# Performance work log

Measured on AMD Instinct MI355X. Metric: run time of the kernel, lower is better.

The kernel has to match this reference:

```python
import jax, jax.numpy as jnp
import numpy as np

N_NODES = 20000
N_EDGES = 320000
IN_DIM = 64        # 18 + 7 + 19 + 20
EDGE_DIM0 = 112    # edge_length of conv1
HID = 50
N_REST = 9         # conv2..conv10
EPS = 1e-5


def setup_inputs() -> dict:
    key = jax.random.key(0)
    ks = jax.random.split(key, 16)
    s = 0.05
    x = jax.random.normal(ks[0], (N_NODES, IN_DIM), jnp.float32)
    edge_index = jax.random.randint(ks[1], (2, N_EDGES), 0, N_NODES, jnp.int32)
    edge_attr = jax.random.normal(ks[2], (N_EDGES, EDGE_DIM0), jnp.float32)
    distance = jax.random.normal(ks[3], (N_EDGES,), jnp.float32)
    d1 = 2 * IN_DIM + EDGE_DIM0       # concat width for layer 1
    dk = 2 * HID + HID                # concat width for layers 2..10
    return {
        "x": x,
        "edge_index": edge_index,
        "edge_attr": edge_attr,
        "distance": distance,
        # layer-1 params (edge-conditioned message MLP + edge-update MLP)
        "W1m": jax.random.normal(ks[4], (d1, HID), jnp.float32) * s,
        "b1m": jnp.zeros((HID,), jnp.float32),
        "W1e": jax.random.normal(ks[5], (d1, HID), jnp.float32) * s,
        "b1e": jnp.zeros((HID,), jnp.float32),
        "g1": jnp.ones((HID,), jnp.float32),
        "bt1": jnp.zeros((HID,), jnp.float32),
        # layers 2..10, stacked
        "Wm": jax.random.normal(ks[6], (N_REST, dk, HID), jnp.float32) * s,
        "bm": jnp.zeros((N_REST, HID), jnp.float32),
        "We": jax.random.normal(ks[7], (N_REST, dk, HID), jnp.float32) * s,
        "be": jnp.zeros((N_REST, HID), jnp.float32),
        "gam": jnp.ones((N_REST, HID), jnp.float32),
        "bet": jnp.zeros((N_REST, HID), jnp.float32),
    }


def reference(x, edge_index, edge_attr, distance,
              W1m, b1m, W1e, b1e, g1, bt1,
              Wm, bm, We, be, gam, bet):
    src = edge_index[0]
    dst = edge_index[1]

    def gcn(xn, ea, Wm_, bm_, We_, be_):
        # gather endpoint features, concat with edge_attr: [E, 2*F + Fe]
        h = jnp.concatenate([xn[dst], xn[src], ea], axis=-1)
        m = h @ Wm_ + bm_                 # per-edge message   [E, HID]
        e_new = h @ We_ + be_             # updated edge_attr  [E, HID]
        xo = jax.ops.segment_sum(m, dst, num_segments=N_NODES)  # scatter-add
        return xo, e_new

    def bn(v, g, b):
        # BatchNorm1d, batch-statistics (training-mode) semantics
        mu = v.mean(0)
        var = ((v - mu) ** 2).mean(0)
        return (v - mu) * jax.lax.rsqrt(var + EPS) * g + b

    x1, e = gcn(x, edge_attr, W1m, b1m, W1e, b1e)
    x1 = jax.nn.elu(bn(x1, g1, bt1))
    cur = x1  # cumulative residual sum x1 + x2 + ... + xk
    for i in range(N_REST):
        xi, e = gcn(cur, e, Wm[i], bm[i], We[i], be[i])
        xi = jax.nn.elu(bn(xi, gam[i], bet[i]))
        cur = cur + xi
    return cur  # x10_C: [N_NODES, HID]
```

## Files before the change

kernel.cpp:

```cpp
#include <hip/hip_runtime.h>
#include <hip/hip_bf16.h>
#include <math.h>

#define N_NODES 20000
#define N_EDGES 320000
#define HID 50
#define XS 64

typedef short bf16x8 __attribute__((ext_vector_type(8)));
typedef float f32x4 __attribute__((ext_vector_type(4)));

__device__ inline ushort f2bf(float f) {
    __hip_bfloat16 h = __float2bfloat16(f);
    union { __hip_bfloat16 h; ushort u; } c; c.h = h; return c.u;
}
__device__ inline uint pack2(float a, float b) {
    return (uint)f2bf(a) | ((uint)f2bf(b) << 16);
}

__device__ inline void lds_barrier() {
    asm volatile("s_waitcnt lgkmcnt(0)" ::: "memory");
    __builtin_amdgcn_sched_barrier(0);
    __builtin_amdgcn_s_barrier();
    __builtin_amdgcn_sched_barrier(0);
    asm volatile("" ::: "memory");
}

__global__ __launch_bounds__(256) void hist_kernel(const int* __restrict__ dst, int* __restrict__ cnt) {
    const int e = blockIdx.x * 256 + threadIdx.x;
    if (e < N_EDGES) atomicAdd(&cnt[dst[e]], 1);
}

__global__ __launch_bounds__(1024) void scan_kernel(const int* __restrict__ cnt, int* __restrict__ offs) {
    __shared__ int part[1024];
    const int t = threadIdx.x;
    int loc[20]; int s = 0;
    #pragma unroll
    for (int i = 0; i < 20; ++i) {
        const int idx = t * 20 + i;
        const int v = (idx < N_NODES) ? cnt[idx] : 0;
        loc[i] = s; s += v;
    }
    part[t] = s; __syncthreads();
    for (int off = 1; off < 1024; off <<= 1) {
        const int v = (t >= off) ? part[t - off] : 0;
        __syncthreads();
        part[t] += v;
        __syncthreads();
    }
    const int ex = (t > 0) ? part[t - 1] : 0;
    #pragma unroll
    for (int i = 0; i < 20; ++i) {
        const int idx = t * 20 + i;
        if (idx < N_NODES) offs[idx] = ex + loc[i];
    }
}

__global__ __launch_bounds__(256) void scatter_kernel(const int* __restrict__ src, const int* __restrict__ dst,
        int* __restrict__ offs, int* __restrict__ perm,
        int* __restrict__ sdst_p, int* __restrict__ ssrc_p) {
    const int e = blockIdx.x * 256 + threadIdx.x;
    if (e >= N_EDGES) return;
    const int d = dst[e];
    const int pos = atomicAdd(&offs[d], 1);
    perm[pos] = e;
    sdst_p[pos] = d;
    ssrc_p[pos] = src[e];
}

__global__ __launch_bounds__(256) void xconv_kernel(const float* __restrict__ x, ushort* __restrict__ xb1) {
    const int i = blockIdx.x * 256 + threadIdx.x;
    if (i < N_NODES * 64) xb1[i] = f2bf(x[i]);
}

__global__ __launch_bounds__(256) void prep_w_kernel(
    const float* __restrict__ Wm, const float* __restrict__ We,
    const float* __restrict__ bm, const float* __restrict__ be,
    ushort* __restrict__ Wt, float* __restrict__ bc, int F, int FE, int Kpad)
{
    const int l = blockIdx.y;
    const int K = 2 * F + FE;
    const float* Wm_l = Wm + (size_t)l * K * HID;
    const float* We_l = We + (size_t)l * K * HID;
    const float* bm_l = bm + (size_t)l * HID;
    const float* be_l = be + (size_t)l * HID;
    ushort* Wt_l = Wt + (size_t)l * 128 * Kpad;
    float*  bc_l = bc + (size_t)l * 128;
    for (int idx = blockIdx.x * 256 + threadIdx.x; idx < 128 * Kpad; idx += gridDim.x * 256) {
        const int c = idx / Kpad;
        const int k = idx - c * Kpad;
        int r = -1;
        if (k < 64)       { if (k < F)        r = k; }
        else if (k < 128) { if (k - 64 < F)   r = F + (k - 64); }
        else              { if (k - 128 < FE) r = 2 * F + (k - 128); }
        float v = 0.f;
        if (r >= 0) {
            if (c < HID)                      v = Wm_l[(size_t)r * HID + c];
            else if (c >= 64 && c < 64 + HID) v = We_l[(size_t)r * HID + (c - 64)];
        }
        Wt_l[(size_t)c * Kpad + k] = f2bf(v);
        if (k == 0) {
            float b = 0.f;
            if (c < HID)                      b = bm_l[c];
            else if (c >= 64 && c < 64 + HID) b = be_l[c - 64];
            bc_l[c] = b;
        }
    }
}

template<int NCH, bool L1>
__global__ __launch_bounds__(256, L1 ? 1 : 4) void msg_mfma_kernel(
    const ushort* __restrict__ xb,
    const float*  __restrict__ ea,
    const ushort* __restrict__ ein,
    const int*    __restrict__ perm,
    ushort* __restrict__ eout,
    const int* __restrict__ sdst_idx, const int* __restrict__ ssrc_idx,
    const ushort* __restrict__ Wt,
    const float* __restrict__ bc,
    float* __restrict__ xo)
{
    constexpr int KPAD = NCH * 32;
    constexpr int KPS  = KPAD + 8;
    constexpr int NT   = N_EDGES / 32;

    __shared__ __align__(16) ushort hl[32 * KPS];
    __shared__ __align__(16) float  xol[32 * 52];
    __shared__ __align__(16) ushort epack[32 * 72];
    __shared__ int sdst_s[2][32];
    __shared__ int segs[34];
    __shared__ int nseg_s;

    const int t = threadIdx.x;
    const int lane = t & 63, w = t >> 6;
    const int r = t >> 3, ch0 = t & 7;
    const int row16 = lane & 15, g = lane >> 4;
    const int G = gridDim.x;

    int sd, ss, pm;
    bf16x8 Rd, Rs, Re;
    float4 P0a, P0b, P1a, P1b;

    auto issue = [&](int tl) {
        const int eb = tl * 32;
        sd = sdst_idx[eb + r];
        ss = ssrc_idx[eb + r];
        Rd = *(const bf16x8*)(xb + (size_t)sd * XS + ch0 * 8);
        Rs = *(const bf16x8*)(xb + (size_t)ss * XS + ch0 * 8);
        if constexpr (L1) {
            pm = perm[eb + r];
            const float* pe = ea + (size_t)pm * 112;
            P0a = *(const float4*)(pe + 8 * ch0);
            P0b = *(const float4*)(pe + 8 * ch0 + 4);
            if (ch0 < 6) {
                P1a = *(const float4*)(pe + 8 * (ch0 + 8));
                P1b = *(const float4*)(pe + 8 * (ch0 + 8) + 4);
            }
        } else {
            Re = *(const bf16x8*)(ein + ((size_t)eb + r) * XS + ch0 * 8);
        }
    };

    auto write_stage = [&](int par) {
        *(bf16x8*)&hl[r * KPS + ch0 * 8]      = Rd;
        *(bf16x8*)&hl[r * KPS + 64 + ch0 * 8] = Rs;
        if constexpr (L1) {
            union { bf16x8 v; uint u[4]; } c0;
            c0.u[0] = pack2(P0a.x, P0a.y); c0.u[1] = pack2(P0a.z, P0a.w);
            c0.u[2] = pack2(P0b.x, P0b.y); c0.u[3] = pack2(P0b.z, P0b.w);
            *(bf16x8*)&hl[r * KPS + 128 + ch0 * 8] = c0.v;
            if (ch0 < 6) {
                union { bf16x8 v; uint u[4]; } c1;
                c1.u[0] = pack2(P1a.x, P1a.y); c1.u[1] = pack2(P1a.z, P1a.w);
                c1.u[2] = pack2(P1b.x, P1b.y); c1.u[3] = pack2(P1b.z, P1b.w);
                *(bf16x8*)&hl[r * KPS + 192 + ch0 * 8] = c1.v;
            } else {
                *(bf16x8*)&hl[r * KPS + 192 + ch0 * 8] = (bf16x8){0,0,0,0,0,0,0,0};
            }
        } else {
            *(bf16x8*)&hl[r * KPS + 128 + ch0 * 8] = Re;
        }
        if (ch0 == 0) sdst_s[par][r] = sd;
    };

    int tile = blockIdx.x;
    if (tile >= NT) return;

    const int colA = (2 * w) * 16 + row16;
    const int colB = colA + 16;
    const float bA = bc[colA], bB = bc[colB];
    const ushort* wpA = Wt + (size_t)colA * KPAD + 8 * g;
    const ushort* wpB = Wt + (size_t)colB * KPAD + 8 * g;

    bf16x8 BfA[NCH], BfB[NCH];
    if constexpr (!L1) {
        #pragma unroll
        for (int c = 0; c < NCH; ++c) {
            BfA[c] = *(const bf16x8*)(wpA + c * 32);
            BfB[c] = *(const bf16x8*)(wpB + c * 32);
        }
    }

    issue(tile);
    write_stage(0);
    if (tile + G < NT) issue(tile + G);
    __syncthreads();

    int par = 0;
    for (; tile < NT; tile += G) {
        f32x4 accA0 = (f32x4){bA, bA, bA, bA}, accA1 = accA0;
        f32x4 accB0 = (f32x4){bB, bB, bB, bB}, accB1 = accB0;
        #pragma unroll
        for (int c = 0; c < NCH; ++c) {
            const bf16x8 a0 = *(const bf16x8*)&hl[row16 * KPS + c * 32 + 8 * g];
            const bf16x8 a1 = *(const bf16x8*)&hl[(16 + row16) * KPS + c * 32 + 8 * g];
            bf16x8 B0, B1;
            if constexpr (L1) {
                B0 = *(const bf16x8*)(wpA + c * 32);
                B1 = *(const bf16x8*)(wpB + c * 32);
            } else {
                B0 = BfA[c];
                B1 = BfB[c];
            }
            accA0 = __builtin_amdgcn_mfma_f32_16x16x32_bf16(a0, B0, accA0, 0, 0, 0);
            accA1 = __builtin_amdgcn_mfma_f32_16x16x32_bf16(a1, B0, accA1, 0, 0, 0);
            accB0 = __builtin_amdgcn_mfma_f32_16x16x32_bf16(a0, B1, accB0, 0, 0, 0);
            accB1 = __builtin_amdgcn_mfma_f32_16x16x32_bf16(a1, B1, accB1, 0, 0, 0);
        }

        if (w < 2) {
            #pragma unroll
            for (int rr = 0; rr < 4; ++rr) {
                if (colA < HID) {
                    xol[(4 * g + rr) * 52 + colA]      = accA0[rr];
                    xol[(16 + 4 * g + rr) * 52 + colA] = accA1[rr];
                }
                if (colB < HID) {
                    xol[(4 * g + rr) * 52 + colB]      = accB0[rr];
                    xol[(16 + 4 * g + rr) * 52 + colB] = accB1[rr];
                }
            }
        } else {
            const int lcA = colA - 64, lcB = colB - 64;
            #pragma unroll
            for (int rr = 0; rr < 4; ++rr) {
                epack[(4 * g + rr) * 72 + lcA]      = f2bf(accA0[rr]);
                epack[(16 + 4 * g + rr) * 72 + lcA] = f2bf(accA1[rr]);
                epack[(4 * g + rr) * 72 + lcB]      = f2bf(accB0[rr]);
                epack[(16 + 4 * g + rr) * 72 + lcB] = f2bf(accB1[rr]);
            }
        }

        if (w == 0) {
            const int l31 = lane & 31;
            const int dl  = sdst_s[par][l31];
            const int dp  = sdst_s[par][l31 > 0 ? l31 - 1 : 0];
            const bool flag = (l31 == 0) || (dl != dp);
            const unsigned long long bal = __ballot(flag) & 0xFFFFFFFFull;
            if (lane < 32 && flag)
                segs[__popcll(bal & ((1ull << l31) - 1ull))] = l31;
            if (lane == 0) {
                const int ns = __popcll(bal);
                nseg_s = ns;
                segs[ns] = 32;
            }
        }
        lds_barrier();

        if (tile + G < NT)     write_stage(par ^ 1);
        if (tile + 2 * G < NT) issue(tile + 2 * G);

        {
            const int4 v = *(const int4*)&epack[r * 72 + ch0 * 8];
            *(int4*)&eout[((size_t)tile * 32 + r) * XS + ch0 * 8] = v;
        }
        const int ns = nseg_s;
        for (int idx = t; idx < ns * HID; idx += 256) {
            const int s = idx / HID, col = idx - s * HID;
            const int a0 = segs[s], b0 = segs[s + 1];
            float s0 = 0.f, s1 = 0.f, s2 = 0.f, s3 = 0.f;
            int rr = a0;
            for (; rr + 4 <= b0; rr += 4) {
                s0 += xol[(rr + 0) * 52 + col];
                s1 += xol[(rr + 1) * 52 + col];
                s2 += xol[(rr + 2) * 52 + col];
                s3 += xol[(rr + 3) * 52 + col];
            }
            for (; rr < b0; ++rr) s0 += xol[rr * 52 + col];
            atomicAdd(&xo[(size_t)sdst_s[par][a0] * HID + col], (s0 + s1) + (s2 + s3));
        }
        lds_barrier();
        par ^= 1;
    }
}

__global__ __launch_bounds__(256) void stats_kernel(const float* __restrict__ xo,
                                                    float* __restrict__ sacc)
{
    __shared__ float sp[5][HID], sq[5][HID];
    const int t = threadIdx.x;
    if (t < 250) {
        float s = 0.f, q = 0.f;
        const size_t base = (size_t)blockIdx.x * 12500 + t;
        #pragma unroll
        for (int it = 0; it < 50; ++it) {
            const float v = xo[base + it * 250];
            s += v; q += v * v;
        }
        sp[t / HID][t % HID] = s;
        sq[t / HID][t % HID] = q;
    }
    __syncthreads();
    if (t < HID) {
        float s = 0.f, q = 0.f;
        #pragma unroll
        for (int p = 0; p < 5; ++p) { s += sp[p][t]; q += sq[p][t]; }
        atomicAdd(&sacc[t], s);
        atomicAdd(&sacc[HID + t], q);
    }
}

template<bool FIRST>
__global__ __launch_bounds__(256) void apply_kernel(float* __restrict__ xo,
    const float* __restrict__ sacc,
    const float* __restrict__ g, const float* __restrict__ b,
    float* __restrict__ cur, ushort* __restrict__ xb)
{
    const int i = blockIdx.x * 256 + threadIdx.x;
    if (i >= N_NODES * HID) return;
    const int c = i % HID;
    const float inv = 1.f / (float)N_NODES;
    const float mu = sacc[c] * inv;
    const float var = sacc[HID + c] * inv - mu * mu;
    const float z = (xo[i] - mu) * rsqrtf(var + 1e-5f) * g[c] + b[c];
    xo[i] = 0.f;
    const float a = (z > 0.f) ? z : expm1f(z);
    const float nc = FIRST ? a : (cur[i] + a);
    cur[i] = nc;
    xb[(size_t)(i / HID) * XS + c] = f2bf(nc);
}

extern "C" void kernel_launch(void* const* d_in, const int* in_sizes, int n_in,
                              void* d_out, int out_size, void* d_ws, size_t ws_size,
                              hipStream_t stream)
{
    const float* x    = (const float*)d_in[0];
    const int*   ei   = (const int*)  d_in[1];
    const float* ea   = (const float*)d_in[2];
    const float* W1m  = (const float*)d_in[4];
    const float* b1m  = (const float*)d_in[5];
    const float* W1e  = (const float*)d_in[6];
    const float* b1e  = (const float*)d_in[7];
    const float* g1   = (const float*)d_in[8];
    const float* bt1  = (const float*)d_in[9];
    const float* Wm   = (const float*)d_in[10];
    const float* bm   = (const float*)d_in[11];
    const float* We   = (const float*)d_in[12];
    const float* be   = (const float*)d_in[13];
    const float* gam  = (const float*)d_in[14];
    const float* bet  = (const float*)d_in[15];

    float* out = (float*)d_out;

    char* ws = (char*)d_ws;
    ushort* e_ws   = (ushort*)(ws + 0);
    float*  xo     = (float*) (ws + 40960000);
    float*  sacc   = (float*) (ws + 44960000);
    ushort* Wt1    = (ushort*)(ws + 44965120);
    float*  bc1    = (float*) (ws + 45030656);
    ushort* Wtk    = (ushort*)(ws + 45031168);
    float*  bck    = (float*) (ws + 45473536);
    ushort* xb1    = (ushort*)(ws + 45478656);
    ushort* xb     = (ushort*)(ws + 48038656);
    int*    cnt    = (int*)   (ws + 50598656);
    int*    offs   = (int*)   (ws + 50678656);
    int*    perm   = (int*)   (ws + 50758656);
    int*    sdst_p = (int*)   (ws + 52038656);
    int*    ssrc_p = (int*)   (ws + 53318656);

    const int* srcs = ei;
    const int* dsts = ei + N_EDGES;
    const int nApply = (N_NODES * HID + 255) / 256;

    hipMemsetAsync(xo, 0, 4005120, stream);
    hipMemsetAsync(xb, 0, 2560000, stream);
    hipMemsetAsync(cnt, 0, N_NODES * sizeof(int), stream);
    hist_kernel<<<1250, 256, 0, stream>>>(dsts, cnt);
    scan_kernel<<<1, 1024, 0, stream>>>(cnt, offs);
    scatter_kernel<<<1250, 256, 0, stream>>>(srcs, dsts, offs, perm, sdst_p, ssrc_p);
    xconv_kernel<<<5000, 256, 0, stream>>>(x, xb1);
    prep_w_kernel<<<dim3(128, 1), 256, 0, stream>>>(W1m, W1e, b1m, b1e, Wt1, bc1, 64, 112, 256);
    prep_w_kernel<<<dim3(128, 9), 256, 0, stream>>>(Wm, We, bm, be, Wtk, bck, 50, 50, 192);

    msg_mfma_kernel<8, true>
        <<<1280, 256, 0, stream>>>(xb1, ea, (const ushort*)nullptr, perm,
                                   e_ws, sdst_p, ssrc_p, Wt1, bc1, xo);
    stats_kernel<<<80, 256, 0, stream>>>(xo, sacc);
    apply_kernel<true><<<nApply, 256, 0, stream>>>(xo, sacc, g1, bt1, out, xb);

    for (int i = 0; i < 9; ++i) {
        msg_mfma_kernel<6, false>
            <<<1024, 256, 0, stream>>>(xb, (const float*)nullptr, e_ws, (const int*)nullptr,
                                       e_ws, sdst_p, ssrc_p,
                                       Wtk + (size_t)i * 128 * 192,
                                       bck + (size_t)i * 128, xo);
        stats_kernel<<<80, 256, 0, stream>>>(xo, sacc + (i + 1) * 128);
        apply_kernel<false><<<nApply, 256, 0, stream>>>(xo, sacc + (i + 1) * 128,
                                                        gam + (size_t)i * HID,
                                                        bet + (size_t)i * HID, out, xb);
    }
}
```

Baseline: 527.0 us.

## Fuse BN stats and apply into one grid-synced kernel; prefetch indices earlier

Merges the BatchNorm statistics and apply kernels into one kernel. Each block caches its slice of the aggregated features in LDS, contributes partial sums, then spins on an atomic counter in the sacc workspace until all 250 blocks arrive, and applies BN+ELU from the cache. This removes one launch per layer and a second global read of xo. The message kernel also splits index loading from the feature gather, so indices are fetched one tile further ahead and their latency is hidden. The spin barrier only works if all 250 blocks are co-resident, and it depends on the counter slot in sacc starting at zero.

```diff
diff --git a/kernel.cpp b/kernel.cpp
--- a/kernel.cpp
+++ b/kernel.cpp
@@ -137,19 +137,23 @@
     const int row16 = lane & 15, g = lane >> 4;
     const int G = gridDim.x;
 
-    int sd, ss, pm;
+    int sdN, ssN, pmN;
+    int sdW;
     bf16x8 Rd, Rs, Re;
     float4 P0a, P0b, P1a, P1b;
 
-    auto issue = [&](int tl) {
+    auto load_idx = [&](int tl) {
         const int eb = tl * 32;
-        sd = sdst_idx[eb + r];
-        ss = ssrc_idx[eb + r];
-        Rd = *(const bf16x8*)(xb + (size_t)sd * XS + ch0 * 8);
-        Rs = *(const bf16x8*)(xb + (size_t)ss * XS + ch0 * 8);
+        sdN = sdst_idx[eb + r];
+        ssN = ssrc_idx[eb + r];
+        if constexpr (L1) pmN = perm[eb + r];
+    };
+
+    auto gather = [&](int tl) {
+        Rd = *(const bf16x8*)(xb + (size_t)sdN * XS + ch0 * 8);
+        Rs = *(const bf16x8*)(xb + (size_t)ssN * XS + ch0 * 8);
         if constexpr (L1) {
-            pm = perm[eb + r];
-            const float* pe = ea + (size_t)pm * 112;
+            const float* pe = ea + (size_t)pmN * 112;
             P0a = *(const float4*)(pe + 8 * ch0);
             P0b = *(const float4*)(pe + 8 * ch0 + 4);
             if (ch0 < 6) {
@@ -157,8 +161,9 @@
                 P1b = *(const float4*)(pe + 8 * (ch0 + 8) + 4);
             }
         } else {
-            Re = *(const bf16x8*)(ein + ((size_t)eb + r) * XS + ch0 * 8);
-        }
+            Re = *(const bf16x8*)(ein + ((size_t)tl * 32 + r) * XS + ch0 * 8);
+        }
+        sdW = sdN;
     };
 
     auto write_stage = [&](int par) {
@@ -180,7 +185,7 @@
         } else {
             *(bf16x8*)&hl[r * KPS + 128 + ch0 * 8] = Re;
         }
-        if (ch0 == 0) sdst_s[par][r] = sd;
+        if (ch0 == 0) sdst_s[par][r] = sdW;
     };
 
     int tile = blockIdx.x;
@@ -201,9 +206,9 @@
         }
     }
 
-    issue(tile);
-    write_stage(0);
-    if (tile + G < NT) issue(tile + G);
+    load_idx(tile); gather(tile); write_stage(0);
+    if (tile + G < NT)     { load_idx(tile + G); gather(tile + G); }
+    if (tile + 2 * G < NT) load_idx(tile + 2 * G);
     __syncthreads();
 
     int par = 0;
@@ -268,7 +273,8 @@
         lds_barrier();
 
         if (tile + G < NT)     write_stage(par ^ 1);
-        if (tile + 2 * G < NT) issue(tile + 2 * G);
+        if (tile + 2 * G < NT) gather(tile + 2 * G);
+        if (tile + 3 * G < NT) load_idx(tile + 3 * G);
 
         {
             const int4 v = *(const int4*)&epack[r * 72 + ch0 * 8];
@@ -294,17 +300,25 @@
     }
 }
 
-__global__ __launch_bounds__(256) void stats_kernel(const float* __restrict__ xo,
-                                                    float* __restrict__ sacc)
+template<bool FIRST>
+__global__ __launch_bounds__(256) void bnapply_kernel(float* __restrict__ xo,
+    float* __restrict__ sacc,
+    const float* __restrict__ g, const float* __restrict__ b,
+    float* __restrict__ cur, ushort* __restrict__ xb)
 {
+    __shared__ float cache[4000];
     __shared__ float sp[5][HID], sq[5][HID];
+    __shared__ float mvs[2 * HID];
+
     const int t = threadIdx.x;
+    const size_t base = (size_t)blockIdx.x * 4000;
+
     if (t < 250) {
         float s = 0.f, q = 0.f;
-        const size_t base = (size_t)blockIdx.x * 12500 + t;
         #pragma unroll
-        for (int it = 0; it < 50; ++it) {
-            const float v = xo[base + it * 250];
+        for (int it = 0; it < 16; ++it) {
+            const float v = xo[base + t + it * 250];
+            cache[t + it * 250] = v;
             s += v; q += v * v;
         }
         sp[t / HID][t % HID] = s;
@@ -318,26 +332,31 @@
         atomicAdd(&sacc[t], s);
         atomicAdd(&sacc[HID + t], q);
     }
-}
-
-template<bool FIRST>
-__global__ __launch_bounds__(256) void apply_kernel(float* __restrict__ xo,
-    const float* __restrict__ sacc,
-    const float* __restrict__ g, const float* __restrict__ b,
-    float* __restrict__ cur, ushort* __restrict__ xb)
-{
-    const int i = blockIdx.x * 256 + threadIdx.x;
-    if (i >= N_NODES * HID) return;
-    const int c = i % HID;
+    __syncthreads();
+
+    if (t == 0) {
+        int* cnt = (int*)(sacc + 112);
+        atomicAdd(cnt, 1);
+        while (atomicAdd(cnt, 0) < 250) { __builtin_amdgcn_s_sleep(8); }
+    }
+    __syncthreads();
+
+    if (t < 2 * HID) mvs[t] = atomicAdd(&sacc[t], 0.0f);
+    __syncthreads();
+
     const float inv = 1.f / (float)N_NODES;
-    const float mu = sacc[c] * inv;
-    const float var = sacc[HID + c] * inv - mu * mu;
-    const float z = (xo[i] - mu) * rsqrtf(var + 1e-5f) * g[c] + b[c];
-    xo[i] = 0.f;
-    const float a = (z > 0.f) ? z : expm1f(z);
-    const float nc = FIRST ? a : (cur[i] + a);
-    cur[i] = nc;
-    xb[(size_t)(i / HID) * XS + c] = f2bf(nc);
+    for (int i = t; i < 4000; i += 256) {
+        const int c = i % HID;
+        const int node = (int)(base / HID) + i / HID;
+        const float mu = mvs[c] * inv;
+        const float var = mvs[HID + c] * inv - mu * mu;
+        const float z = (cache[i] - mu) * rsqrtf(var + 1e-5f) * g[c] + b[c];
+        xo[base + i] = 0.f;
+        const float a = (z > 0.f) ? z : expm1f(z);
+        const float nc = FIRST ? a : (cur[base + i] + a);
+        cur[base + i] = nc;
+        xb[(size_t)node * XS + c] = f2bf(nc);
+    }
 }
 
 extern "C" void kernel_launch(void* const* d_in, const int* in_sizes, int n_in,
@@ -380,7 +399,6 @@
 
     const int* srcs = ei;
     const int* dsts = ei + N_EDGES;
-    const int nApply = (N_NODES * HID + 255) / 256;
 
     hipMemsetAsync(xo, 0, 4005120, stream);
     hipMemsetAsync(xb, 0, 2560000, stream);
@@ -395,8 +413,7 @@
     msg_mfma_kernel<8, true>
         <<<1280, 256, 0, stream>>>(xb1, ea, (const ushort*)nullptr, perm,
                                    e_ws, sdst_p, ssrc_p, Wt1, bc1, xo);
-    stats_kernel<<<80, 256, 0, stream>>>(xo, sacc);
-    apply_kernel<true><<<nApply, 256, 0, stream>>>(xo, sacc, g1, bt1, out, xb);
+    bnapply_kernel<true><<<250, 256, 0, stream>>>(xo, sacc, g1, bt1, out, xb);
 
     for (int i = 0; i < 9; ++i) {
         msg_mfma_kernel<6, false>
@@ -404,9 +421,8 @@
                                        e_ws, sdst_p, ssrc_p,
                                        Wtk + (size_t)i * 128 * 192,
                                        bck + (size_t)i * 128, xo);
-        stats_kernel<<<80, 256, 0, stream>>>(xo, sacc + (i + 1) * 128);
-        apply_kernel<false><<<nApply, 256, 0, stream>>>(xo, sacc + (i + 1) * 128,
-                                                        gam + (size_t)i * HID,
-                                                        bet + (size_t)i * HID, out, xb);
-    }
-}
+        bnapply_kernel<false><<<250, 256, 0, stream>>>(xo, sacc + (i + 1) * 128,
+                                                       gam + (size_t)i * HID,
+                                                       bet + (size_t)i * HID, out, xb);
+    }
+}
```

Result: slower. 654.0 us (+24.1%).

## Generalize edge tile size and use 64-edge tiles for layers 2-10

Applied to the files above, without the earlier changes.

Templates the message kernel on edges-per-tile so each block processes 64 edges per iteration in layers 2-10, with four M-subtiles of MFMA per B fragment and a full-wave ballot for segment detection. This reuses register-resident weights across more rows, halves per-tile barrier and loop overhead, and lets segments of equal destination span more edges so fewer atomics are issued. It also drops the occupancy hint from launch bounds and lowers the grid to 768 blocks. In exchange it raises LDS and register use per block, which may reduce occupancy, and doubles the in-flight gather registers.

```diff
diff --git a/kernel.cpp b/kernel.cpp
--- a/kernel.cpp
+++ b/kernel.cpp
@@ -108,8 +108,8 @@
     }
 }
 
-template<int NCH, bool L1>
-__global__ __launch_bounds__(256, L1 ? 1 : 4) void msg_mfma_kernel(
+template<int NCH, int ET, bool L1>
+__global__ __launch_bounds__(256) void msg_mfma_kernel(
     const ushort* __restrict__ xb,
     const float*  __restrict__ ea,
     const ushort* __restrict__ ein,
@@ -122,13 +122,15 @@
 {
     constexpr int KPAD = NCH * 32;
     constexpr int KPS  = KPAD + 8;
-    constexpr int NT   = N_EDGES / 32;
-
-    __shared__ __align__(16) ushort hl[32 * KPS];
-    __shared__ __align__(16) float  xol[32 * 52];
-    __shared__ __align__(16) ushort epack[32 * 72];
-    __shared__ int sdst_s[2][32];
-    __shared__ int segs[34];
+    constexpr int NT   = N_EDGES / ET;
+    constexpr int MT   = ET / 16;
+    constexpr int NR   = ET / 32;
+
+    __shared__ __align__(16) ushort hl[ET * KPS];
+    __shared__ __align__(16) float  xol[ET * 52];
+    __shared__ __align__(16) ushort epack[ET * 72];
+    __shared__ int sdst_s[2][ET];
+    __shared__ int segs[ET + 2];
     __shared__ int nseg_s;
 
     const int t = threadIdx.x;
@@ -137,50 +139,60 @@
     const int row16 = lane & 15, g = lane >> 4;
     const int G = gridDim.x;
 
-    int sd, ss, pm;
-    bf16x8 Rd, Rs, Re;
+    int sd[NR], ss[NR], pm[NR];
+    bf16x8 Rd[NR], Rs[NR], Re[NR];
     float4 P0a, P0b, P1a, P1b;
 
     auto issue = [&](int tl) {
-        const int eb = tl * 32;
-        sd = sdst_idx[eb + r];
-        ss = ssrc_idx[eb + r];
-        Rd = *(const bf16x8*)(xb + (size_t)sd * XS + ch0 * 8);
-        Rs = *(const bf16x8*)(xb + (size_t)ss * XS + ch0 * 8);
-        if constexpr (L1) {
-            pm = perm[eb + r];
-            const float* pe = ea + (size_t)pm * 112;
-            P0a = *(const float4*)(pe + 8 * ch0);
-            P0b = *(const float4*)(pe + 8 * ch0 + 4);
-            if (ch0 < 6) {
-                P1a = *(const float4*)(pe + 8 * (ch0 + 8));
-                P1b = *(const float4*)(pe + 8 * (ch0 + 8) + 4);
-            }
-        } else {
-            Re = *(const bf16x8*)(ein + ((size_t)eb + r) * XS + ch0 * 8);
+        #pragma unroll
+        for (int i = 0; i < NR; ++i) {
+            const int eb = tl * ET + i * 32;
+            sd[i] = sdst_idx[eb + r];
+            ss[i] = ssrc_idx[eb + r];
+            if constexpr (L1) pm[i] = perm[eb + r];
+        }
+        #pragma unroll
+        for (int i = 0; i < NR; ++i) {
+            Rd[i] = *(const bf16x8*)(xb + (size_t)sd[i] * XS + ch0 * 8);
+            Rs[i] = *(const bf16x8*)(xb + (size_t)ss[i] * XS + ch0 * 8);
+            if constexpr (L1) {
+                const float* pe = ea + (size_t)pm[i] * 112;
+                P0a = *(const float4*)(pe + 8 * ch0);
+                P0b = *(const float4*)(pe + 8 * ch0 + 4);
+                if (ch0 < 6) {
+                    P1a = *(const float4*)(pe + 8 * (ch0 + 8));
+                    P1b = *(const float4*)(pe + 8 * (ch0 + 8) + 4);
+                }
+            } else {
+                Re[i] = *(const bf16x8*)(ein + ((size_t)tl * ET + i * 32 + r) * XS + ch0 * 8);
+            }
         }
     };
 
     auto write_stage = [&](int par) {
-        *(bf16x8*)&hl[r * KPS + ch0 * 8]      = Rd;
-        *(bf16x8*)&hl[r * KPS + 64 + ch0 * 8] = Rs;
-        if constexpr (L1) {
-            union { bf16x8 v; uint u[4]; } c0;
-            c0.u[0] = pack2(P0a.x, P0a.y); c0.u[1] = pack2(P0a.z, P0a.w);
-            c0.u[2] = pack2(P0b.x, P0b.y); c0.u[3] = pack2(P0b.z, P0b.w);
-            *(bf16x8*)&hl[r * KPS + 128 + ch0 * 8] = c0.v;
-            if (ch0 < 6) {
-                union { bf16x8 v; uint u[4]; } c1;
-                c1.u[0] = pack2(P1a.x, P1a.y); c1.u[1] = pack2(P1a.z, P1a.w);
-                c1.u[2] = pack2(P1b.x, P1b.y); c1.u[3] = pack2(P1b.z, P1b.w);
-                *(bf16x8*)&hl[r * KPS + 192 + ch0 * 8] = c1.v;
+        #pragma unroll
+        for (int i = 0; i < NR; ++i) {
+            const int row = r + i * 32;
+            *(bf16x8*)&hl[row * KPS + ch0 * 8]      = Rd[i];
+            *(bf16x8*)&hl[row * KPS + 64 + ch0 * 8] = Rs[i];
+            if constexpr (L1) {
+                union { bf16x8 v; uint u[4]; } c0;
+                c0.u[0] = pack2(P0a.x, P0a.y); c0.u[1] = pack2(P0a.z, P0a.w);
+                c0.u[2] = pack2(P0b.x, P0b.y); c0.u[3] = pack2(P0b.z, P0b.w);
+                *(bf16x8*)&hl[row * KPS + 128 + ch0 * 8] = c0.v;
+                if (ch0 < 6) {
+                    union { bf16x8 v; uint u[4]; } c1;
+                    c1.u[0] = pack2(P1a.x, P1a.y); c1.u[1] = pack2(P1a.z, P1a.w);
+                    c1.u[2] = pack2(P1b.x, P1b.y); c1.u[3] = pack2(P1b.z, P1b.w);
+                    *(bf16x8*)&hl[row * KPS + 192 + ch0 * 8] = c1.v;
+                } else {
+                    *(bf16x8*)&hl[row * KPS + 192 + ch0 * 8] = (bf16x8){0,0,0,0,0,0,0,0};
+                }
             } else {
-                *(bf16x8*)&hl[r * KPS + 192 + ch0 * 8] = (bf16x8){0,0,0,0,0,0,0,0};
-            }
-        } else {
-            *(bf16x8*)&hl[r * KPS + 128 + ch0 * 8] = Re;
-        }
-        if (ch0 == 0) sdst_s[par][r] = sd;
+                *(bf16x8*)&hl[row * KPS + 128 + ch0 * 8] = Re[i];
+            }
+            if (ch0 == 0) sdst_s[par][row] = sd[i];
+        }
     };
 
     int tile = blockIdx.x;
@@ -208,12 +220,18 @@
 
     int par = 0;
     for (; tile < NT; tile += G) {
-        f32x4 accA0 = (f32x4){bA, bA, bA, bA}, accA1 = accA0;
-        f32x4 accB0 = (f32x4){bB, bB, bB, bB}, accB1 = accB0;
+        f32x4 accA[MT], accB[MT];
+        #pragma unroll
+        for (int m = 0; m < MT; ++m) {
+            accA[m] = (f32x4){bA, bA, bA, bA};
+            accB[m] = (f32x4){bB, bB, bB, bB};
+        }
         #pragma unroll
         for (int c = 0; c < NCH; ++c) {
-            const bf16x8 a0 = *(const bf16x8*)&hl[row16 * KPS + c * 32 + 8 * g];
-            const bf16x8 a1 = *(const bf16x8*)&hl[(16 + row16) * KPS + c * 32 + 8 * g];
+            bf16x8 a[MT];
+            #pragma unroll
+            for (int m = 0; m < MT; ++m)
+                a[m] = *(const bf16x8*)&hl[(m * 16 + row16) * KPS + c * 32 + 8 * g];
             bf16x8 B0, B1;
             if constexpr (L1) {
                 B0 = *(const bf16x8*)(wpA + c * 32);
@@ -222,47 +240,61 @@
                 B0 = BfA[c];
                 B1 = BfB[c];
             }
-            accA0 = __builtin_amdgcn_mfma_f32_16x16x32_bf16(a0, B0, accA0, 0, 0, 0);
-            accA1 = __builtin_amdgcn_mfma_f32_16x16x32_bf16(a1, B0, accA1, 0, 0, 0);
-            accB0 = __builtin_amdgcn_mfma_f32_16x16x32_bf16(a0, B1, accB0, 0, 0, 0);
-            accB1 = __builtin_amdgcn_mfma_f32_16x16x32_bf16(a1, B1, accB1, 0, 0, 0);
+            #pragma unroll
+            for (int m = 0; m < MT; ++m) {
+                accA[m] = __builtin_amdgcn_mfma_f32_16x16x32_bf16(a[m], B0, accA[m], 0, 0, 0);
+                accB[m] = __builtin_amdgcn_mfma_f32_16x16x32_bf16(a[m], B1, accB[m], 0, 0, 0);
+            }
         }
 
         if (w < 2) {
             #pragma unroll
-            for (int rr = 0; rr < 4; ++rr) {
-                if (colA < HID) {
-                    xol[(4 * g + rr) * 52 + colA]      = accA0[rr];
-                    xol[(16 + 4 * g + rr) * 52 + colA] = accA1[rr];
-                }
-                if (colB < HID) {
-                    xol[(4 * g + rr) * 52 + colB]      = accB0[rr];
-                    xol[(16 + 4 * g + rr) * 52 + colB] = accB1[rr];
+            for (int m = 0; m < MT; ++m) {
+                #pragma unroll
+                for (int rr = 0; rr < 4; ++rr) {
+                    const int row = m * 16 + 4 * g + rr;
+                    if (colA < HID) xol[row * 52 + colA] = accA[m][rr];
+                    if (colB < HID) xol[row * 52 + colB] = accB[m][rr];
                 }
             }
         } else {
             const int lcA = colA - 64, lcB = colB - 64;
             #pragma unroll
-            for (int rr = 0; rr < 4; ++rr) {
-                epack[(4 * g + rr) * 72 + lcA]      = f2bf(accA0[rr]);
-                epack[(16 + 4 * g + rr) * 72 + lcA] = f2bf(accA1[rr]);
-                epack[(4 * g + rr) * 72 + lcB]      = f2bf(accB0[rr]);
-                epack[(16 + 4 * g + rr) * 72 + lcB] = f2bf(accB1[rr]);
+            for (int m = 0; m < MT; ++m) {
+                #pragma unroll
+                for (int rr = 0; rr < 4; ++rr) {
+                    const int row = m * 16 + 4 * g + rr;
+                    epack[row * 72 + lcA] = f2bf(accA[m][rr]);
+                    epack[row * 72 + lcB] = f2bf(accB[m][rr]);
+                }
             }
         }
 
         if (w == 0) {
-            const int l31 = lane & 31;
-            const int dl  = sdst_s[par][l31];
-            const int dp  = sdst_s[par][l31 > 0 ? l31 - 1 : 0];
-            const bool flag = (l31 == 0) || (dl != dp);
-            const unsigned long long bal = __ballot(flag) & 0xFFFFFFFFull;
-            if (lane < 32 && flag)
-                segs[__popcll(bal & ((1ull << l31) - 1ull))] = l31;
-            if (lane == 0) {
-                const int ns = __popcll(bal);
-                nseg_s = ns;
-                segs[ns] = 32;
+            if constexpr (ET == 64) {
+                const int dl = sdst_s[par][lane];
+                const int dp = sdst_s[par][lane > 0 ? lane - 1 : 0];
+                const bool flag = (lane == 0) || (dl != dp);
+                const unsigned long long bal = __ballot(flag);
+                if (flag) segs[__popcll(bal & ((1ull << lane) - 1ull))] = lane;
+                if (lane == 63) {
+                    const int ns = __popcll(bal);
+                    nseg_s = ns;
+                    segs[ns] = 64;
+                }
+            } else {
+                const int l31 = lane & 31;
+                const int dl  = sdst_s[par][l31];
+                const int dp  = sdst_s[par][l31 > 0 ? l31 - 1 : 0];
+                const bool flag = (l31 == 0) || (dl != dp);
+                const unsigned long long bal = __ballot(flag) & 0xFFFFFFFFull;
+                if (lane < 32 && flag)
+                    segs[__popcll(bal & ((1ull << l31) - 1ull))] = l31;
+                if (lane == 0) {
+                    const int ns = __popcll(bal);
+                    nseg_s = ns;
+                    segs[ns] = 32;
+                }
             }
         }
         lds_barrier();
@@ -270,9 +302,11 @@
         if (tile + G < NT)     write_stage(par ^ 1);
         if (tile + 2 * G < NT) issue(tile + 2 * G);
 
-        {
-            const int4 v = *(const int4*)&epack[r * 72 + ch0 * 8];
-            *(int4*)&eout[((size_t)tile * 32 + r) * XS + ch0 * 8] = v;
+        #pragma unroll
+        for (int i = 0; i < NR; ++i) {
+            const int row = r + i * 32;
+            const int4 v = *(const int4*)&epack[row * 72 + ch0 * 8];
+            *(int4*)&eout[((size_t)tile * ET + row) * XS + ch0 * 8] = v;
         }
         const int ns = nseg_s;
         for (int idx = t; idx < ns * HID; idx += 256) {
@@ -392,18 +426,18 @@
     prep_w_kernel<<<dim3(128, 1), 256, 0, stream>>>(W1m, W1e, b1m, b1e, Wt1, bc1, 64, 112, 256);
     prep_w_kernel<<<dim3(128, 9), 256, 0, stream>>>(Wm, We, bm, be, Wtk, bck, 50, 50, 192);
 
-    msg_mfma_kernel<8, true>
+    msg_mfma_kernel<8, 32, true>
         <<<1280, 256, 0, stream>>>(xb1, ea, (const ushort*)nullptr, perm,
                                    e_ws, sdst_p, ssrc_p, Wt1, bc1, xo);
     stats_kernel<<<80, 256, 0, stream>>>(xo, sacc);
     apply_kernel<true><<<nApply, 256, 0, stream>>>(xo, sacc, g1, bt1, out, xb);
 
     for (int i = 0; i < 9; ++i) {
-        msg_mfma_kernel<6, false>
-            <<<1024, 256, 0, stream>>>(xb, (const float*)nullptr, e_ws, (const int*)nullptr,
-                                       e_ws, sdst_p, ssrc_p,
-                                       Wtk + (size_t)i * 128 * 192,
-                                       bck + (size_t)i * 128, xo);
+        msg_mfma_kernel<6, 64, false>
+            <<<768, 256, 0, stream>>>(xb, (const float*)nullptr, e_ws, (const int*)nullptr,
+                                      e_ws, sdst_p, ssrc_p,
+                                      Wtk + (size_t)i * 128 * 192,
+                                      bck + (size_t)i * 128, xo);
         stats_kernel<<<80, 256, 0, stream>>>(xo, sacc + (i + 1) * 128);
         apply_kernel<false><<<nApply, 256, 0, stream>>>(xo, sacc + (i + 1) * 128,
                                                         gam + (size_t)i * HID,
```

After: 654.5 us. +24.2%, slower.
